# Performance work log

Hardware: AMD Instinct MI355X
Metric: run time of the kernel (lower is better)

Reference implementation:

```python
import jax, jax.numpy as jnp
import numpy as np

HEAD = 8
DIM_HEAD = 64
EPS = 1e-5  # torch GroupNorm default


def group_norm(x, w, b, groups, eps=EPS):
    # x: [B, C, H, W]; normalize per (group, spatial)
    B, C, H, W = x.shape
    xg = x.reshape(B, groups, C // groups, H, W)
    mu = xg.mean(axis=(2, 3, 4), keepdims=True)
    var = xg.var(axis=(2, 3, 4), keepdims=True)
    xn = ((xg - mu) / jnp.sqrt(var + eps)).reshape(B, C, H, W)
    return xn * w[None, :, None, None] + b[None, :, None, None]


def setup_inputs() -> dict:
    key = jax.random.key(0)
    ks = jax.random.split(key, 4)
    dim = 256
    hidden = HEAD * DIM_HEAD  # 512
    x = jax.random.normal(ks[0], (16, dim, 64, 64), dtype=jnp.float32)
    qkv_w = jax.random.normal(ks[1], (hidden * 3, dim), dtype=jnp.float32) * 0.02
    out_w = jax.random.normal(ks[2], (dim, hidden), dtype=jnp.float32) * 0.02
    out_b = jnp.zeros((dim,), dtype=jnp.float32)
    gn1_w = jnp.ones((dim,), dtype=jnp.float32)
    gn1_b = jnp.zeros((dim,), dtype=jnp.float32)
    gn2_w = jnp.ones((dim,), dtype=jnp.float32)
    gn2_b = jnp.zeros((dim,), dtype=jnp.float32)
    return {"x": x, "gn1_w": gn1_w, "gn1_b": gn1_b, "qkv_w": qkv_w,
            "out_w": out_w, "out_b": out_b, "gn2_w": gn2_w, "gn2_b": gn2_b}


def reference(x, gn1_w, gn1_b, qkv_w, out_w, out_b, gn2_w, gn2_b):
    B, C, I, J = x.shape
    groups = C // 8
    scale = DIM_HEAD ** -0.5
    n = I * J

    xn = group_norm(x, gn1_w, gn1_b, groups)
    # 1x1 conv == channel matmul: [B,3*hidden,I,J]
    qkv = jnp.einsum('bchw,oc->bohw', xn, qkv_w)
    q, k, v = jnp.split(qkv, 3, axis=1)

    def to_heads(t):  # [B, h*f, I, J] -> [B, h, f, n]
        return t.reshape(B, HEAD, DIM_HEAD, n)

    q = jax.nn.softmax(to_heads(q), axis=-2) * scale  # softmax over feature dim
    k = jax.nn.softmax(to_heads(k), axis=-1)          # softmax over spatial dim
    v = to_heads(v)

    context = jnp.einsum('bhfm,bhem->bhfe', k, v)     # [B,h,f,e]
    attn = jnp.einsum('bhfe,bhfn->bhen', context, q)  # [B,h,e,n]
    out = attn.reshape(B, HEAD * DIM_HEAD, I, J)

    out = jnp.einsum('bchw,oc->bohw', out, out_w) + out_b[None, :, None, None]
    return group_norm(out, gn2_w, gn2_b, groups)
```

## Files before the change

kernel.cpp:

```cpp
#include <hip/hip_runtime.h>
#include <math.h>

#define NB   16
#define NC   256
#define NP   4096
#define NHD  8
#define FD   64
#define HID  512
#define OC3  1536
#define NG   32
#define CPG  8
#define GEPS 1e-5f

typedef __attribute__((ext_vector_type(8))) short bf16x8;
typedef __attribute__((ext_vector_type(4))) float f32x4;

#define MFMA_BF16(a, b, c) __builtin_amdgcn_mfma_f32_16x16x32_bf16(a, b, c, 0, 0, 0)

__device__ __forceinline__ uint bf16_rne(float v) {
    uint u = __float_as_uint(v);
    return (u + 0x7FFFu + ((u >> 16) & 1u)) >> 16;
}
__device__ __forceinline__ void split2(float v, uint& h, uint& l) {
    h = bf16_rne(v);
    l = bf16_rne(v - __uint_as_float(h << 16));
}
__device__ __forceinline__ void gload16(const void* g, void* l) {
    __builtin_amdgcn_global_load_lds(
        (const __attribute__((address_space(1))) void*)g,
        (__attribute__((address_space(3))) void*)l, 16, 0, 0);
}

__global__ __launch_bounds__(256) void gn_stats_kernel(const float* __restrict__ x,
                                                       float* __restrict__ mu,
                                                       float* __restrict__ rstd) {
    int bg = blockIdx.x;
    const float4* b4 = (const float4*)(x + (size_t)bg * CPG * NP);
    int t = threadIdx.x;
    float s = 0.f, sq = 0.f;
    #pragma unroll
    for (int i = 0; i < 32; ++i) {
        float4 v = b4[t + i * 256];
        s  += v.x + v.y + v.z + v.w;
        sq += v.x*v.x + v.y*v.y + v.z*v.z + v.w*v.w;
    }
    for (int off = 32; off; off >>= 1) { s += __shfl_down(s, off); sq += __shfl_down(sq, off); }
    __shared__ float ss[4], ssq[4];
    int wid = t >> 6, lane = t & 63;
    if (lane == 0) { ss[wid] = s; ssq[wid] = sq; }
    __syncthreads();
    if (t == 0) {
        float S  = ss[0] + ss[1] + ss[2] + ss[3];
        float SQ = ssq[0] + ssq[1] + ssq[2] + ssq[3];
        const float inv = 1.f / (float)(CPG * NP);
        float m = S * inv;
        float var = SQ * inv - m * m;
        mu[bg] = m;
        rstd[bg] = rsqrtf(var + GEPS);
    }
}

__global__ void gn1_coefs_kernel(const float* __restrict__ mu, const float* __restrict__ rstd,
                                 const float* __restrict__ w, const float* __restrict__ bias,
                                 float* __restrict__ ac, float* __restrict__ dc) {
    int i = blockIdx.x * 256 + threadIdx.x;
    if (i >= NB * NC) return;
    int b = i / NC, c = i % NC;
    int g = c / CPG;
    float m = mu[b * NG + g], r = rstd[b * NG + g];
    float a = r * w[c];
    ac[i] = a;
    dc[i] = bias[c] - m * a;
}

__global__ void wsplit_kernel(const float* __restrict__ w, ushort* __restrict__ wh,
                              ushort* __restrict__ wl) {
    int i = blockIdx.x * 256 + threadIdx.x;
    float4 v = ((const float4*)w)[i];
    uint h, l;
    ushort4 hv, lv;
    split2(v.x, h, l); hv.x = (ushort)h; lv.x = (ushort)l;
    split2(v.y, h, l); hv.y = (ushort)h; lv.y = (ushort)l;
    split2(v.z, h, l); hv.z = (ushort)h; lv.z = (ushort)l;
    split2(v.w, h, l); hv.w = (ushort)h; lv.w = (ushort)l;
    ((ushort4*)wh)[i] = hv;
    ((ushort4*)wl)[i] = lv;
}

__global__ __launch_bounds__(256) void xsplit_kernel(const float* __restrict__ x,
                                                     const float* __restrict__ ac,
                                                     const float* __restrict__ dc,
                                                     ushort* __restrict__ xTh,
                                                     ushort* __restrict__ xTl, int b0) {
    int z = blockIdx.z, bglob = b0 + z;
    int p0 = blockIdx.x * 64, c0 = blockIdx.y * 64;
    const float* xb = x + (size_t)bglob * NC * NP;
    __shared__ float T[64][72];
    int t = threadIdx.x;
    #pragma unroll
    for (int j = 0; j < 4; ++j) {
        int idx = t + j * 256;
        int r = idx >> 4, c4 = idx & 15;
        float4 v = *(const float4*)(xb + (size_t)(c0 + r) * NP + p0 + c4 * 4);
        float a = ac[bglob * NC + c0 + r], d = dc[bglob * NC + c0 + r];
        v.x = fmaf(v.x, a, d); v.y = fmaf(v.y, a, d);
        v.z = fmaf(v.z, a, d); v.w = fmaf(v.w, a, d);
        *(float4*)&T[r][c4 * 4] = v;
    }
    __syncthreads();
    int p = t >> 2, cseg = t & 3;
    size_t ob = ((size_t)z * NP + p0 + p) * NC + c0 + cseg * 16;
    #pragma unroll
    for (int half = 0; half < 2; ++half) {
        uint4 uh, ul;
        uint* ph = (uint*)&uh; uint* pl = (uint*)&ul;
        #pragma unroll
        for (int i = 0; i < 4; ++i) {
            int c = cseg * 16 + half * 8 + i * 2;
            uint h0, l0, h1, l1;
            split2(T[c][p], h0, l0);
            split2(T[c + 1][p], h1, l1);
            ph[i] = h0 | (h1 << 16);
            pl[i] = l0 | (l1 << 16);
        }
        *(uint4*)(xTh + ob + half * 8) = uh;
        *(uint4*)(xTl + ob + half * 8) = ul;
    }
}

__global__ __launch_bounds__(256) void gemm_q_kernel(
        const ushort* __restrict__ Ah, const ushort* __restrict__ Al,
        const ushort* __restrict__ Bhg, const ushort* __restrict__ Blg,
        ushort* __restrict__ qsTh) {
    __shared__ __align__(16) char smem[33280];
    const int z = blockIdx.z;
    const ushort* Bh = Bhg + (size_t)NP * NC * z;
    const ushort* Bl = Blg + (size_t)NP * NC * z;

    const int t = threadIdx.x;
    const int w = t >> 6, l = t & 63;
    const int wr = w >> 1, wc = w & 1;
    const int m0 = blockIdx.y * 128, n0 = blockIdx.x * 128;
    const int l15 = l & 15, kb = l >> 4;

    f32x4 acc[4][4];
    #pragma unroll
    for (int i = 0; i < 4; ++i)
        #pragma unroll
        for (int j = 0; j < 4; ++j)
            acc[i][j] = (f32x4){0.f, 0.f, 0.f, 0.f};

    for (int k0 = 0; k0 < NC; k0 += 32) {
        #pragma unroll
        for (int j = 0; j < 2; ++j) {
            int idx = t + j * 256;
            int m = idx & 127, s = idx >> 7;
            size_t goA = (size_t)(m0 + m) * NC + k0 + s * 8;
            size_t goB = (size_t)(n0 + m) * NC + k0 + s * 8;
            int lo = idx * 16;
            gload16(Ah + goA, smem + lo);
            gload16(Al + goA, smem + 8192 + lo);
            gload16(Bh + goB, smem + 16384 + lo);
            gload16(Bl + goB, smem + 24576 + lo);
        }
        __syncthreads();
        bf16x8 ah[4], al[4];
        #pragma unroll
        for (int fi = 0; fi < 4; ++fi) {
            int off = (kb * 128 + wr * 64 + fi * 16 + l15) * 16;
            ah[fi] = *(const bf16x8*)(smem + off);
            al[fi] = *(const bf16x8*)(smem + 8192 + off);
        }
        #pragma unroll
        for (int fj = 0; fj < 4; ++fj) {
            int off = (kb * 128 + wc * 64 + fj * 16 + l15) * 16;
            bf16x8 bh = *(const bf16x8*)(smem + 16384 + off);
            bf16x8 bl = *(const bf16x8*)(smem + 24576 + off);
            #pragma unroll
            for (int fi = 0; fi < 4; ++fi) {
                acc[fi][fj] = MFMA_BF16(ah[fi], bh, acc[fi][fj]);
                acc[fi][fj] = MFMA_BF16(al[fi], bh, acc[fi][fj]);
                acc[fi][fj] = MFMA_BF16(ah[fi], bl, acc[fi][fj]);
            }
        }
        __syncthreads();
    }

    uint* Tq = (uint*)smem;
    #pragma unroll
    for (int half = 0; half < 2; ++half) {
        if (wc == half) {
            #pragma unroll
            for (int fj = 0; fj < 4; ++fj) {
                float ex[16];
                float cs = 0.f;
                #pragma unroll
                for (int fi = 0; fi < 4; ++fi)
                    #pragma unroll
                    for (int r = 0; r < 4; ++r) {
                        float e = __expf(acc[fi][fj][r]);
                        ex[fi * 4 + r] = e;
                        cs += e;
                    }
                cs += __shfl_xor(cs, 16);
                cs += __shfl_xor(cs, 32);
                float inv = 0.125f / cs;
                int p_loc = fj * 16 + l15;
                #pragma unroll
                for (int fi = 0; fi < 4; ++fi)
                    #pragma unroll
                    for (int r = 0; r < 4; ++r) {
                        uint hb = bf16_rne(ex[fi * 4 + r] * inv);
                        Tq[p_loc * 130 + wr * 64 + fi * 16 + kb * 4 + r] = hb << 16;
                    }
            }
        }
        __syncthreads();
        int p = t >> 2, seg = t & 3;
        size_t ob = ((size_t)z * NP + n0 + half * 64 + p) * HID + m0 + seg * 32;
        #pragma unroll
        for (int c = 0; c < 4; ++c) {
            uint4 H;
            uint* hp = (uint*)&H;
            #pragma unroll
            for (int i = 0; i < 4; ++i) {
                uint u0 = Tq[p * 130 + seg * 32 + c * 8 + 2 * i];
                uint u1 = Tq[p * 130 + seg * 32 + c * 8 + 2 * i + 1];
                hp[i] = (u0 >> 16) | (u1 & 0xffff0000u);
            }
            *(uint4*)(qsTh + ob + c * 8) = H;
        }
        __syncthreads();
    }
}

__global__ __launch_bounds__(512, 4) void kv_ctx_kernel(
        const ushort* __restrict__ Wh, const ushort* __restrict__ Wl,
        const ushort* __restrict__ Bhg, const ushort* __restrict__ Blg,
        float* __restrict__ ctxp, float* __restrict__ kspart) {
    __shared__ __align__(16) char smem[69632];
    const int z = blockIdx.z;
    const int h = blockIdx.y;
    const int tile = blockIdx.x;
    const int n0 = tile * 128;
    const ushort* Bh = Bhg + (size_t)NP * NC * z;
    const ushort* Bl = Blg + (size_t)NP * NC * z;

    const int t = threadIdx.x;
    const int w = t >> 6, l = t & 63;
    const int wr = w >> 2, wc = w & 3;
    const int l15 = l & 15, kb = l >> 4;

    ushort* ekh = (ushort*)smem;
    ushort* ekl = ekh + 64 * 136;
    ushort* vh_ = ekl + 64 * 136;
    ushort* vl_ = vh_ + 64 * 136;

    f32x4 acc[4][2];
    #pragma unroll
    for (int i = 0; i < 4; ++i)
        #pragma unroll
        for (int j = 0; j < 2; ++j)
            acc[i][j] = (f32x4){0.f, 0.f, 0.f, 0.f};

    for (int k0 = 0; k0 < NC; k0 += 32) {
        {
            int idx = t;
            int m = idx & 127, s = idx >> 7;
            int grow = 512 + h * 64 + (m & 63) + ((m >> 6) << 9);
            size_t goA = (size_t)grow * NC + k0 + s * 8;
            size_t goB = (size_t)(n0 + m) * NC + k0 + s * 8;
            int lo = idx * 16;
            gload16(Wh + goA, smem + lo);
            gload16(Wl + goA, smem + 8192 + lo);
            gload16(Bh + goB, smem + 16384 + lo);
            gload16(Bl + goB, smem + 24576 + lo);
        }
        __syncthreads();
        bf16x8 ah[4], al[4];
        #pragma unroll
        for (int fi = 0; fi < 4; ++fi) {
            int off = (kb * 128 + wr * 64 + fi * 16 + l15) * 16;
            ah[fi] = *(const bf16x8*)(smem + off);
            al[fi] = *(const bf16x8*)(smem + 8192 + off);
        }
        #pragma unroll
        for (int fj = 0; fj < 2; ++fj) {
            int off = (kb * 128 + wc * 32 + fj * 16 + l15) * 16;
            bf16x8 bh = *(const bf16x8*)(smem + 16384 + off);
            bf16x8 bl = *(const bf16x8*)(smem + 24576 + off);
            #pragma unroll
            for (int fi = 0; fi < 4; ++fi) {
                acc[fi][fj] = MFMA_BF16(ah[fi], bh, acc[fi][fj]);
                acc[fi][fj] = MFMA_BF16(al[fi], bh, acc[fi][fj]);
                acc[fi][fj] = MFMA_BF16(ah[fi], bl, acc[fi][fj]);
            }
        }
        __syncthreads();
    }

    #pragma unroll
    for (int fi = 0; fi < 4; ++fi) {
        #pragma unroll
        for (int r = 0; r < 4; ++r) {
            int row = fi * 16 + kb * 4 + r;
            float rs = 0.f;
            #pragma unroll
            for (int fj = 0; fj < 2; ++fj) {
                float v = acc[fi][fj][r];
                float e = (wr == 0) ? __expf(v) : v;
                rs += e;
                uint hb, lb;
                split2(e, hb, lb);
                int P = wc * 32 + fj * 16 + l15;
                if (wr == 0) { ekh[row * 136 + P] = (ushort)hb; ekl[row * 136 + P] = (ushort)lb; }
                else         { vh_[row * 136 + P] = (ushort)hb; vl_[row * 136 + P] = (ushort)lb; }
            }
            if (wr == 0) {
                rs += __shfl_xor(rs, 1); rs += __shfl_xor(rs, 2);
                rs += __shfl_xor(rs, 4); rs += __shfl_xor(rs, 8);
                if (l15 == 0)
                    kspart[((size_t)z * HID + h * 64 + row) * 128 + tile * 4 + wc] = rs;
            }
        }
    }
    __syncthreads();

    f32x4 c2[2];
    c2[0] = (f32x4){0.f, 0.f, 0.f, 0.f};
    c2[1] = (f32x4){0.f, 0.f, 0.f, 0.f};
    const int cr0 = (w >> 2) * 32;
    const int cc0 = (w & 3) * 16;
    #pragma unroll
    for (int ks = 0; ks < 4; ++ks) {
        bf16x8 a_h[2], a_l[2];
        #pragma unroll
        for (int i = 0; i < 2; ++i) {
            int offa = (cr0 + i * 16 + l15) * 136 + ks * 32 + kb * 8;
            a_h[i] = *(const bf16x8*)(ekh + offa);
            a_l[i] = *(const bf16x8*)(ekl + offa);
        }
        int offb = (cc0 + l15) * 136 + ks * 32 + kb * 8;
        bf16x8 b_h = *(const bf16x8*)(vh_ + offb);
        bf16x8 b_l = *(const bf16x8*)(vl_ + offb);
        #pragma unroll
        for (int i = 0; i < 2; ++i) {
            c2[i] = MFMA_BF16(a_h[i], b_h, c2[i]);
            c2[i] = MFMA_BF16(a_l[i], b_h, c2[i]);
            c2[i] = MFMA_BF16(a_h[i], b_l, c2[i]);
        }
    }
    float* outp = ctxp + (((size_t)z * NHD + h) * 32 + tile) * 4096;
    #pragma unroll
    for (int i = 0; i < 2; ++i)
        #pragma unroll
        for (int r = 0; r < 4; ++r)
            outp[(size_t)(cr0 + i * 16 + kb * 4 + r) * 64 + cc0 + l15] = c2[i][r];
}

__global__ void ksum_reduce_kernel(const float* __restrict__ kspart,
                                   float* __restrict__ ksum, int n) {
    int i = blockIdx.x * 256 + threadIdx.x;
    if (i >= n) return;
    float s = 0.f;
    #pragma unroll
    for (int j = 0; j < 128; ++j) s += kspart[(size_t)i * 128 + j];
    ksum[i] = s;
}

__global__ __launch_bounds__(256) void fold_kernel(const float* __restrict__ out_w,
                                                   const float* __restrict__ ctxp,
                                                   const float* __restrict__ ksum,
                                                   ushort* __restrict__ w2h,
                                                   ushort* __restrict__ w2l) {
    int h = blockIdx.x, z = blockIdx.y;
    __shared__ float Cs[FD][FD];
    int t = threadIdx.x;
    const float* pbase = ctxp + ((size_t)z * NHD + h) * 32 * 4096;
    #pragma unroll
    for (int j = 0; j < 16; ++j) {
        int idx = t + j * 256;
        float s = 0.f;
        #pragma unroll
        for (int p8 = 0; p8 < 32; ++p8) s += pbase[(size_t)p8 * 4096 + idx];
        ((float*)Cs)[idx] = s;
    }
    __syncthreads();
    float wr[64];
    const float* wrow = out_w + (size_t)t * HID + h * FD;
    #pragma unroll
    for (int e = 0; e < 64; ++e) wr[e] = wrow[e];
    size_t ob = ((size_t)z * NC + t) * HID + h * FD;
    for (int f = 0; f < 64; ++f) {
        float sacc = 0.f;
        #pragma unroll
        for (int e = 0; e < 64; ++e) sacc = fmaf(wr[e], Cs[f][e], sacc);
        float v = sacc / ksum[(size_t)z * HID + h * FD + f];
        uint hb, lb;
        split2(v, hb, lb);
        w2h[ob + f] = (ushort)hb;
        w2l[ob + f] = (ushort)lb;
    }
}

__global__ __launch_bounds__(256) void gemm_out_kernel(
        const ushort* __restrict__ Ahg, const ushort* __restrict__ Alg,
        const ushort* __restrict__ Bhg,
        const float* __restrict__ bias, float* __restrict__ outg,
        float2* __restrict__ gn2part, int b0) {
    __shared__ __align__(16) char smem[24576];
    const int z = blockIdx.z, bglob = b0 + z;
    const ushort* Ah = Ahg + (size_t)NC * HID * z;
    const ushort* Al = Alg + (size_t)NC * HID * z;
    const ushort* Bh = Bhg + (size_t)NP * HID * z;
    float* C = outg + (size_t)bglob * NC * NP;

    const int t = threadIdx.x;
    const int w = t >> 6, l = t & 63;
    const int wr = w >> 1, wc = w & 1;
    const int m0 = blockIdx.y * 128, n0 = blockIdx.x * 128;
    const int l15 = l & 15, kb = l >> 4;

    f32x4 acc[4][4];
    #pragma unroll
    for (int i = 0; i < 4; ++i)
        #pragma unroll
        for (int j = 0; j < 4; ++j)
            acc[i][j] = (f32x4){0.f, 0.f, 0.f, 0.f};

    for (int k0 = 0; k0 < HID; k0 += 32) {
        #pragma unroll
        for (int j = 0; j < 2; ++j) {
            int idx = t + j * 256;
            int m = idx & 127, s = idx >> 7;
            size_t goA = (size_t)(m0 + m) * HID + k0 + s * 8;
            size_t goB = (size_t)(n0 + m) * HID + k0 + s * 8;
            int lo = idx * 16;
            gload16(Ah + goA, smem + lo);
            gload16(Al + goA, smem + 8192 + lo);
            gload16(Bh + goB, smem + 16384 + lo);
        }
        __syncthreads();
        bf16x8 ah[4], al[4];
        #pragma unroll
        for (int fi = 0; fi < 4; ++fi) {
            int off = (kb * 128 + wr * 64 + fi * 16 + l15) * 16;
            ah[fi] = *(const bf16x8*)(smem + off);
            al[fi] = *(const bf16x8*)(smem + 8192 + off);
        }
        #pragma unroll
        for (int fj = 0; fj < 4; ++fj) {
            int off = (kb * 128 + wc * 64 + fj * 16 + l15) * 16;
            bf16x8 bh = *(const bf16x8*)(smem + 16384 + off);
            #pragma unroll
            for (int fi = 0; fi < 4; ++fi) {
                acc[fi][fj] = MFMA_BF16(ah[fi], bh, acc[fi][fj]);
                acc[fi][fj] = MFMA_BF16(al[fi], bh, acc[fi][fj]);
            }
        }
        __syncthreads();
    }

    float gs[4] = {0.f, 0.f, 0.f, 0.f}, gq[4] = {0.f, 0.f, 0.f, 0.f};
    #pragma unroll
    for (int fi = 0; fi < 4; ++fi) {
        int mbase = m0 + wr * 64 + fi * 16 + kb * 4;
        #pragma unroll
        for (int fj = 0; fj < 4; ++fj) {
            int n = n0 + wc * 64 + fj * 16 + l15;
            #pragma unroll
            for (int r = 0; r < 4; ++r) {
                float v = acc[fi][fj][r] + bias[mbase + r];
                C[(size_t)(mbase + r) * NP + n] = v;
                gs[fi] += v;
                gq[fi] += v * v;
            }
        }
    }
    #pragma unroll
    for (int fi = 0; fi < 4; ++fi) {
        #pragma unroll
        for (int d = 1; d <= 16; d <<= 1) {
            gs[fi] += __shfl_xor(gs[fi], d);
            gq[fi] += __shfl_xor(gq[fi], d);
        }
    }
    if (l15 == 0 && (kb & 1) == 0) {
        #pragma unroll
        for (int fi = 0; fi < 4; ++fi) {
            int g = ((m0 + wr * 64) >> 3) + fi * 2 + (kb >> 1);
            float2 pv; pv.x = gs[fi]; pv.y = gq[fi];
            gn2part[(((size_t)bglob * NG + g) << 6) + blockIdx.x * 2 + wc] = pv;
        }
    }
}

__global__ void gn2_reduce_kernel(const float2* __restrict__ gn2part,
                                  float* __restrict__ mu, float* __restrict__ rstd) {
    int i = blockIdx.x * 256 + threadIdx.x;
    if (i >= NB * NG) return;
    float s = 0.f, q = 0.f;
    #pragma unroll
    for (int j = 0; j < 64; ++j) {
        float2 p = gn2part[((size_t)i << 6) + j];
        s += p.x; q += p.y;
    }
    const float inv = 1.f / (float)(CPG * NP);
    float m = s * inv;
    float var = q * inv - m * m;
    mu[i] = m;
    rstd[i] = rsqrtf(var + GEPS);
}

__global__ void gn2_apply_kernel(float* __restrict__ out, const float* __restrict__ mu,
                                 const float* __restrict__ rstd, const float* __restrict__ w,
                                 const float* __restrict__ bias) {
    int i = blockIdx.x * 256 + threadIdx.x;
    float4* p = (float4*)out;
    float4 v = p[i];
    size_t e0 = (size_t)i * 4;
    int cidx = (int)((e0 / NP) % NC);
    int bg   = (int)(e0 / ((size_t)CPG * NP));
    float m = mu[bg], r = rstd[bg];
    float a = r * w[cidx];
    float d = bias[cidx] - m * a;
    v.x = fmaf(v.x, a, d); v.y = fmaf(v.y, a, d);
    v.z = fmaf(v.z, a, d); v.w = fmaf(v.w, a, d);
    p[i] = v;
}

extern "C" void kernel_launch(void* const* d_in, const int* in_sizes, int n_in,
                              void* d_out, int out_size, void* d_ws, size_t ws_size,
                              hipStream_t stream) {
    const float* x     = (const float*)d_in[0];
    const float* gn1_w = (const float*)d_in[1];
    const float* gn1_b = (const float*)d_in[2];
    const float* qkv_w = (const float*)d_in[3];
    const float* out_w = (const float*)d_in[4];
    const float* out_b = (const float*)d_in[5];
    const float* gn2_w = (const float*)d_in[6];
    const float* gn2_b = (const float*)d_in[7];
    float* out = (float*)d_out;

    auto need = [](int cb) -> size_t {
        size_t tot = 0;
        auto al = [&](size_t b) { tot = (tot + b + 255) & ~(size_t)255; };
        al((size_t)cb * NP * NC * 2);  al((size_t)cb * NP * NC * 2);
        al((size_t)cb * NP * HID * 2);
        al((size_t)cb * NHD * 32 * FD * FD * 4);
        al((size_t)cb * HID * 128 * 4);
        al((size_t)cb * HID * 4);
        al((size_t)cb * NC * HID * 2); al((size_t)cb * NC * HID * 2);
        al((size_t)OC3 * NC * 2); al((size_t)OC3 * NC * 2);
        al((size_t)2 * NB * NC * 4);
        al((size_t)4 * NB * NG * 4);
        al((size_t)NB * NG * 64 * 8);
        return tot;
    };
    int CB = 1;
    {
        const int cands[5] = {16, 8, 4, 2, 1};
        for (int i = 0; i < 5; ++i) if (need(cands[i]) <= ws_size) { CB = cands[i]; break; }
    }

    char* base = (char*)d_ws;
    size_t off = 0;
    auto carve = [&](size_t b) -> char* {
        char* p = base + off;
        off = (off + b + 255) & ~(size_t)255;
        return p;
    };
    ushort* xTh  = (ushort*)carve((size_t)CB * NP * NC * 2);
    ushort* xTl  = (ushort*)carve((size_t)CB * NP * NC * 2);
    ushort* qsTh = (ushort*)carve((size_t)CB * NP * HID * 2);
    float*  ctxp = (float*) carve((size_t)CB * NHD * 32 * FD * FD * 4);
    float*  kspart = (float*)carve((size_t)CB * HID * 128 * 4);
    float*  ksum = (float*) carve((size_t)CB * HID * 4);
    ushort* w2h  = (ushort*)carve((size_t)CB * NC * HID * 2);
    ushort* w2l  = (ushort*)carve((size_t)CB * NC * HID * 2);
    ushort* Wqh  = (ushort*)carve((size_t)OC3 * NC * 2);
    ushort* Wql  = (ushort*)carve((size_t)OC3 * NC * 2);
    float*  ac   = (float*) carve((size_t)2 * NB * NC * 4);
    float*  dc   = ac + (size_t)NB * NC;
    float*  mu1  = (float*) carve((size_t)4 * NB * NG * 4);
    float*  rstd1 = mu1 + NB * NG;
    float*  mu2   = rstd1 + NB * NG;
    float*  rstd2 = mu2 + NB * NG;
    float2* gn2part = (float2*)carve((size_t)NB * NG * 64 * 8);

    gn_stats_kernel<<<NB * NG, 256, 0, stream>>>(x, mu1, rstd1);
    gn1_coefs_kernel<<<16, 256, 0, stream>>>(mu1, rstd1, gn1_w, gn1_b, ac, dc);
    wsplit_kernel<<<OC3 * NC / 1024, 256, 0, stream>>>(qkv_w, Wqh, Wql);

    for (int b0 = 0; b0 < NB; b0 += CB) {
        xsplit_kernel<<<dim3(NP / 64, NC / 64, CB), 256, 0, stream>>>(x, ac, dc, xTh, xTl, b0);
        kv_ctx_kernel<<<dim3(NP / 128, NHD, CB), 512, 0, stream>>>(Wqh, Wql, xTh, xTl, ctxp, kspart);
        ksum_reduce_kernel<<<(CB * HID + 255) / 256, 256, 0, stream>>>(kspart, ksum, CB * HID);
        gemm_q_kernel<<<dim3(NP / 128, 4, CB), 256, 0, stream>>>(Wqh, Wql, xTh, xTl, qsTh);
        fold_kernel<<<dim3(NHD, CB), 256, 0, stream>>>(out_w, ctxp, ksum, w2h, w2l);
        gemm_out_kernel<<<dim3(NP / 128, 2, CB), 256, 0, stream>>>(
            w2h, w2l, qsTh, out_b, out, gn2part, b0);
    }

    gn2_reduce_kernel<<<2, 256, 0, stream>>>(gn2part, mu2, rstd2);
    gn2_apply_kernel<<<16384, 256, 0, stream>>>(out, mu2, rstd2, gn2_w, gn2_b);
}
```

Before: 487.4 us.

## Merge Q projection GEMM into the KV context kernel as extra grid blocks

Removes the separate gemm_q_kernel launch and folds its work into the kv_ctx kernel: blocks with blockIdx.y >= NHD compute the Q projection plus feature softmax, the rest compute K/V context. The Q path is restructured to 512 threads with 128x128 tiles and one epilogue pass instead of two halves, with the smem row stride changed to 136. This cuts a launch and lets Q and KV work share one grid, improving fill. The cost is that the Q path now runs under the 512-thread, 4-block launch bounds and the larger shared-memory footprint of the KV kernel.

```diff
diff --git a/kernel.cpp b/kernel.cpp
--- a/kernel.cpp
+++ b/kernel.cpp
@@ -128,119 +128,13 @@
     }
 }
 
-__global__ __launch_bounds__(256) void gemm_q_kernel(
-        const ushort* __restrict__ Ah, const ushort* __restrict__ Al,
-        const ushort* __restrict__ Bhg, const ushort* __restrict__ Blg,
-        ushort* __restrict__ qsTh) {
-    __shared__ __align__(16) char smem[33280];
-    const int z = blockIdx.z;
-    const ushort* Bh = Bhg + (size_t)NP * NC * z;
-    const ushort* Bl = Blg + (size_t)NP * NC * z;
-
-    const int t = threadIdx.x;
-    const int w = t >> 6, l = t & 63;
-    const int wr = w >> 1, wc = w & 1;
-    const int m0 = blockIdx.y * 128, n0 = blockIdx.x * 128;
-    const int l15 = l & 15, kb = l >> 4;
-
-    f32x4 acc[4][4];
-    #pragma unroll
-    for (int i = 0; i < 4; ++i)
-        #pragma unroll
-        for (int j = 0; j < 4; ++j)
-            acc[i][j] = (f32x4){0.f, 0.f, 0.f, 0.f};
-
-    for (int k0 = 0; k0 < NC; k0 += 32) {
-        #pragma unroll
-        for (int j = 0; j < 2; ++j) {
-            int idx = t + j * 256;
-            int m = idx & 127, s = idx >> 7;
-            size_t goA = (size_t)(m0 + m) * NC + k0 + s * 8;
-            size_t goB = (size_t)(n0 + m) * NC + k0 + s * 8;
-            int lo = idx * 16;
-            gload16(Ah + goA, smem + lo);
-            gload16(Al + goA, smem + 8192 + lo);
-            gload16(Bh + goB, smem + 16384 + lo);
-            gload16(Bl + goB, smem + 24576 + lo);
-        }
-        __syncthreads();
-        bf16x8 ah[4], al[4];
-        #pragma unroll
-        for (int fi = 0; fi < 4; ++fi) {
-            int off = (kb * 128 + wr * 64 + fi * 16 + l15) * 16;
-            ah[fi] = *(const bf16x8*)(smem + off);
-            al[fi] = *(const bf16x8*)(smem + 8192 + off);
-        }
-        #pragma unroll
-        for (int fj = 0; fj < 4; ++fj) {
-            int off = (kb * 128 + wc * 64 + fj * 16 + l15) * 16;
-            bf16x8 bh = *(const bf16x8*)(smem + 16384 + off);
-            bf16x8 bl = *(const bf16x8*)(smem + 24576 + off);
-            #pragma unroll
-            for (int fi = 0; fi < 4; ++fi) {
-                acc[fi][fj] = MFMA_BF16(ah[fi], bh, acc[fi][fj]);
-                acc[fi][fj] = MFMA_BF16(al[fi], bh, acc[fi][fj]);
-                acc[fi][fj] = MFMA_BF16(ah[fi], bl, acc[fi][fj]);
-            }
-        }
-        __syncthreads();
-    }
-
-    uint* Tq = (uint*)smem;
-    #pragma unroll
-    for (int half = 0; half < 2; ++half) {
-        if (wc == half) {
-            #pragma unroll
-            for (int fj = 0; fj < 4; ++fj) {
-                float ex[16];
-                float cs = 0.f;
-                #pragma unroll
-                for (int fi = 0; fi < 4; ++fi)
-                    #pragma unroll
-                    for (int r = 0; r < 4; ++r) {
-                        float e = __expf(acc[fi][fj][r]);
-                        ex[fi * 4 + r] = e;
-                        cs += e;
-                    }
-                cs += __shfl_xor(cs, 16);
-                cs += __shfl_xor(cs, 32);
-                float inv = 0.125f / cs;
-                int p_loc = fj * 16 + l15;
-                #pragma unroll
-                for (int fi = 0; fi < 4; ++fi)
-                    #pragma unroll
-                    for (int r = 0; r < 4; ++r) {
-                        uint hb = bf16_rne(ex[fi * 4 + r] * inv);
-                        Tq[p_loc * 130 + wr * 64 + fi * 16 + kb * 4 + r] = hb << 16;
-                    }
-            }
-        }
-        __syncthreads();
-        int p = t >> 2, seg = t & 3;
-        size_t ob = ((size_t)z * NP + n0 + half * 64 + p) * HID + m0 + seg * 32;
-        #pragma unroll
-        for (int c = 0; c < 4; ++c) {
-            uint4 H;
-            uint* hp = (uint*)&H;
-            #pragma unroll
-            for (int i = 0; i < 4; ++i) {
-                uint u0 = Tq[p * 130 + seg * 32 + c * 8 + 2 * i];
-                uint u1 = Tq[p * 130 + seg * 32 + c * 8 + 2 * i + 1];
-                hp[i] = (u0 >> 16) | (u1 & 0xffff0000u);
-            }
-            *(uint4*)(qsTh + ob + c * 8) = H;
-        }
-        __syncthreads();
-    }
-}
-
-__global__ __launch_bounds__(512, 4) void kv_ctx_kernel(
+__global__ __launch_bounds__(512, 4) void kvq_kernel(
         const ushort* __restrict__ Wh, const ushort* __restrict__ Wl,
         const ushort* __restrict__ Bhg, const ushort* __restrict__ Blg,
-        float* __restrict__ ctxp, float* __restrict__ kspart) {
+        float* __restrict__ ctxp, float* __restrict__ kspart,
+        ushort* __restrict__ qsTh) {
     __shared__ __align__(16) char smem[69632];
     const int z = blockIdx.z;
-    const int h = blockIdx.y;
     const int tile = blockIdx.x;
     const int n0 = tile * 128;
     const ushort* Bh = Bhg + (size_t)NP * NC * z;
@@ -251,11 +145,6 @@
     const int wr = w >> 2, wc = w & 3;
     const int l15 = l & 15, kb = l >> 4;
 
-    ushort* ekh = (ushort*)smem;
-    ushort* ekl = ekh + 64 * 136;
-    ushort* vh_ = ekl + 64 * 136;
-    ushort* vl_ = vh_ + 64 * 136;
-
     f32x4 acc[4][2];
     #pragma unroll
     for (int i = 0; i < 4; ++i)
@@ -263,99 +152,185 @@
         for (int j = 0; j < 2; ++j)
             acc[i][j] = (f32x4){0.f, 0.f, 0.f, 0.f};
 
-    for (int k0 = 0; k0 < NC; k0 += 32) {
-        {
-            int idx = t;
-            int m = idx & 127, s = idx >> 7;
-            int grow = 512 + h * 64 + (m & 63) + ((m >> 6) << 9);
-            size_t goA = (size_t)grow * NC + k0 + s * 8;
-            size_t goB = (size_t)(n0 + m) * NC + k0 + s * 8;
-            int lo = idx * 16;
-            gload16(Wh + goA, smem + lo);
-            gload16(Wl + goA, smem + 8192 + lo);
-            gload16(Bh + goB, smem + 16384 + lo);
-            gload16(Bl + goB, smem + 24576 + lo);
+    if (blockIdx.y < NHD) {
+        const int h = blockIdx.y;
+        ushort* ekh = (ushort*)smem;
+        ushort* ekl = ekh + 64 * 136;
+        ushort* vh_ = ekl + 64 * 136;
+        ushort* vl_ = vh_ + 64 * 136;
+
+        for (int k0 = 0; k0 < NC; k0 += 32) {
+            {
+                int idx = t;
+                int m = idx & 127, s = idx >> 7;
+                int grow = 512 + h * 64 + (m & 63) + ((m >> 6) << 9);
+                size_t goA = (size_t)grow * NC + k0 + s * 8;
+                size_t goB = (size_t)(n0 + m) * NC + k0 + s * 8;
+                int lo = idx * 16;
+                gload16(Wh + goA, smem + lo);
+                gload16(Wl + goA, smem + 8192 + lo);
+                gload16(Bh + goB, smem + 16384 + lo);
+                gload16(Bl + goB, smem + 24576 + lo);
+            }
+            __syncthreads();
+            bf16x8 ah[4], al[4];
+            #pragma unroll
+            for (int fi = 0; fi < 4; ++fi) {
+                int off = (kb * 128 + wr * 64 + fi * 16 + l15) * 16;
+                ah[fi] = *(const bf16x8*)(smem + off);
+                al[fi] = *(const bf16x8*)(smem + 8192 + off);
+            }
+            #pragma unroll
+            for (int fj = 0; fj < 2; ++fj) {
+                int off = (kb * 128 + wc * 32 + fj * 16 + l15) * 16;
+                bf16x8 bh = *(const bf16x8*)(smem + 16384 + off);
+                bf16x8 bl = *(const bf16x8*)(smem + 24576 + off);
+                #pragma unroll
+                for (int fi = 0; fi < 4; ++fi) {
+                    acc[fi][fj] = MFMA_BF16(ah[fi], bh, acc[fi][fj]);
+                    acc[fi][fj] = MFMA_BF16(al[fi], bh, acc[fi][fj]);
+                    acc[fi][fj] = MFMA_BF16(ah[fi], bl, acc[fi][fj]);
+                }
+            }
+            __syncthreads();
+        }
+
+        #pragma unroll
+        for (int fi = 0; fi < 4; ++fi) {
+            #pragma unroll
+            for (int r = 0; r < 4; ++r) {
+                int row = fi * 16 + kb * 4 + r;
+                float rs = 0.f;
+                #pragma unroll
+                for (int fj = 0; fj < 2; ++fj) {
+                    float v = acc[fi][fj][r];
+                    float e = (wr == 0) ? __expf(v) : v;
+                    rs += e;
+                    uint hb, lb;
+                    split2(e, hb, lb);
+                    int P = wc * 32 + fj * 16 + l15;
+                    if (wr == 0) { ekh[row * 136 + P] = (ushort)hb; ekl[row * 136 + P] = (ushort)lb; }
+                    else         { vh_[row * 136 + P] = (ushort)hb; vl_[row * 136 + P] = (ushort)lb; }
+                }
+                if (wr == 0) {
+                    rs += __shfl_xor(rs, 1); rs += __shfl_xor(rs, 2);
+                    rs += __shfl_xor(rs, 4); rs += __shfl_xor(rs, 8);
+                    if (l15 == 0)
+                        kspart[((size_t)z * HID + h * 64 + row) * 128 + tile * 4 + wc] = rs;
+                }
+            }
         }
         __syncthreads();
-        bf16x8 ah[4], al[4];
-        #pragma unroll
-        for (int fi = 0; fi < 4; ++fi) {
-            int off = (kb * 128 + wr * 64 + fi * 16 + l15) * 16;
-            ah[fi] = *(const bf16x8*)(smem + off);
-            al[fi] = *(const bf16x8*)(smem + 8192 + off);
-        }
+
+        f32x4 c2[2];
+        c2[0] = (f32x4){0.f, 0.f, 0.f, 0.f};
+        c2[1] = (f32x4){0.f, 0.f, 0.f, 0.f};
+        const int cr0 = (w >> 2) * 32;
+        const int cc0 = (w & 3) * 16;
+        #pragma unroll
+        for (int ks = 0; ks < 4; ++ks) {
+            bf16x8 a_h[2], a_l[2];
+            #pragma unroll
+            for (int i = 0; i < 2; ++i) {
+                int offa = (cr0 + i * 16 + l15) * 136 + ks * 32 + kb * 8;
+                a_h[i] = *(const bf16x8*)(ekh + offa);
+                a_l[i] = *(const bf16x8*)(ekl + offa);
+            }
+            int offb = (cc0 + l15) * 136 + ks * 32 + kb * 8;
+            bf16x8 b_h = *(const bf16x8*)(vh_ + offb);
+            bf16x8 b_l = *(const bf16x8*)(vl_ + offb);
+            #pragma unroll
+            for (int i = 0; i < 2; ++i) {
+                c2[i] = MFMA_BF16(a_h[i], b_h, c2[i]);
+                c2[i] = MFMA_BF16(a_l[i], b_h, c2[i]);
+                c2[i] = MFMA_BF16(a_h[i], b_l, c2[i]);
+            }
+        }
+        float* outp = ctxp + (((size_t)z * NHD + h) * 32 + tile) * 4096;
+        #pragma unroll
+        for (int i = 0; i < 2; ++i)
+            #pragma unroll
+            for (int r = 0; r < 4; ++r)
+                outp[(size_t)(cr0 + i * 16 + kb * 4 + r) * 64 + cc0 + l15] = c2[i][r];
+    } else {
+        const int m0 = (blockIdx.y - NHD) * 128;
+
+        for (int k0 = 0; k0 < NC; k0 += 32) {
+            {
+                int idx = t;
+                int m = idx & 127, s = idx >> 7;
+                size_t goA = (size_t)(m0 + m) * NC + k0 + s * 8;
+                size_t goB = (size_t)(n0 + m) * NC + k0 + s * 8;
+                int lo = idx * 16;
+                gload16(Wh + goA, smem + lo);
+                gload16(Wl + goA, smem + 8192 + lo);
+                gload16(Bh + goB, smem + 16384 + lo);
+                gload16(Bl + goB, smem + 24576 + lo);
+            }
+            __syncthreads();
+            bf16x8 ah[4], al[4];
+            #pragma unroll
+            for (int fi = 0; fi < 4; ++fi) {
+                int off = (kb * 128 + wr * 64 + fi * 16 + l15) * 16;
+                ah[fi] = *(const bf16x8*)(smem + off);
+                al[fi] = *(const bf16x8*)(smem + 8192 + off);
+            }
+            #pragma unroll
+            for (int fj = 0; fj < 2; ++fj) {
+                int off = (kb * 128 + wc * 32 + fj * 16 + l15) * 16;
+                bf16x8 bh = *(const bf16x8*)(smem + 16384 + off);
+                bf16x8 bl = *(const bf16x8*)(smem + 24576 + off);
+                #pragma unroll
+                for (int fi = 0; fi < 4; ++fi) {
+                    acc[fi][fj] = MFMA_BF16(ah[fi], bh, acc[fi][fj]);
+                    acc[fi][fj] = MFMA_BF16(al[fi], bh, acc[fi][fj]);
+                    acc[fi][fj] = MFMA_BF16(ah[fi], bl, acc[fi][fj]);
+                }
+            }
+            __syncthreads();
+        }
+
+        uint* Tq = (uint*)smem;
         #pragma unroll
         for (int fj = 0; fj < 2; ++fj) {
-            int off = (kb * 128 + wc * 32 + fj * 16 + l15) * 16;
-            bf16x8 bh = *(const bf16x8*)(smem + 16384 + off);
-            bf16x8 bl = *(const bf16x8*)(smem + 24576 + off);
-            #pragma unroll
-            for (int fi = 0; fi < 4; ++fi) {
-                acc[fi][fj] = MFMA_BF16(ah[fi], bh, acc[fi][fj]);
-                acc[fi][fj] = MFMA_BF16(al[fi], bh, acc[fi][fj]);
-                acc[fi][fj] = MFMA_BF16(ah[fi], bl, acc[fi][fj]);
-            }
+            float ex[16];
+            float cs = 0.f;
+            #pragma unroll
+            for (int fi = 0; fi < 4; ++fi)
+                #pragma unroll
+                for (int r = 0; r < 4; ++r) {
+                    float e = __expf(acc[fi][fj][r]);
+                    ex[fi * 4 + r] = e;
+                    cs += e;
+                }
+            cs += __shfl_xor(cs, 16);
+            cs += __shfl_xor(cs, 32);
+            float inv = 0.125f / cs;
+            int p_loc = wc * 32 + fj * 16 + l15;
+            #pragma unroll
+            for (int fi = 0; fi < 4; ++fi)
+                #pragma unroll
+                for (int r = 0; r < 4; ++r) {
+                    uint hb = bf16_rne(ex[fi * 4 + r] * inv);
+                    Tq[p_loc * 136 + wr * 64 + fi * 16 + kb * 4 + r] = hb << 16;
+                }
         }
         __syncthreads();
-    }
-
-    #pragma unroll
-    for (int fi = 0; fi < 4; ++fi) {
-        #pragma unroll
-        for (int r = 0; r < 4; ++r) {
-            int row = fi * 16 + kb * 4 + r;
-            float rs = 0.f;
-            #pragma unroll
-            for (int fj = 0; fj < 2; ++fj) {
-                float v = acc[fi][fj][r];
-                float e = (wr == 0) ? __expf(v) : v;
-                rs += e;
-                uint hb, lb;
-                split2(e, hb, lb);
-                int P = wc * 32 + fj * 16 + l15;
-                if (wr == 0) { ekh[row * 136 + P] = (ushort)hb; ekl[row * 136 + P] = (ushort)lb; }
-                else         { vh_[row * 136 + P] = (ushort)hb; vl_[row * 136 + P] = (ushort)lb; }
-            }
-            if (wr == 0) {
-                rs += __shfl_xor(rs, 1); rs += __shfl_xor(rs, 2);
-                rs += __shfl_xor(rs, 4); rs += __shfl_xor(rs, 8);
-                if (l15 == 0)
-                    kspart[((size_t)z * HID + h * 64 + row) * 128 + tile * 4 + wc] = rs;
-            }
-        }
-    }
-    __syncthreads();
-
-    f32x4 c2[2];
-    c2[0] = (f32x4){0.f, 0.f, 0.f, 0.f};
-    c2[1] = (f32x4){0.f, 0.f, 0.f, 0.f};
-    const int cr0 = (w >> 2) * 32;
-    const int cc0 = (w & 3) * 16;
-    #pragma unroll
-    for (int ks = 0; ks < 4; ++ks) {
-        bf16x8 a_h[2], a_l[2];
-        #pragma unroll
-        for (int i = 0; i < 2; ++i) {
-            int offa = (cr0 + i * 16 + l15) * 136 + ks * 32 + kb * 8;
-            a_h[i] = *(const bf16x8*)(ekh + offa);
-            a_l[i] = *(const bf16x8*)(ekl + offa);
-        }
-        int offb = (cc0 + l15) * 136 + ks * 32 + kb * 8;
-        bf16x8 b_h = *(const bf16x8*)(vh_ + offb);
-        bf16x8 b_l = *(const bf16x8*)(vl_ + offb);
-        #pragma unroll
-        for (int i = 0; i < 2; ++i) {
-            c2[i] = MFMA_BF16(a_h[i], b_h, c2[i]);
-            c2[i] = MFMA_BF16(a_l[i], b_h, c2[i]);
-            c2[i] = MFMA_BF16(a_h[i], b_l, c2[i]);
-        }
-    }
-    float* outp = ctxp + (((size_t)z * NHD + h) * 32 + tile) * 4096;
-    #pragma unroll
-    for (int i = 0; i < 2; ++i)
-        #pragma unroll
-        for (int r = 0; r < 4; ++r)
-            outp[(size_t)(cr0 + i * 16 + kb * 4 + r) * 64 + cc0 + l15] = c2[i][r];
+        int p = t >> 2, seg = t & 3;
+        size_t ob = ((size_t)z * NP + n0 + p) * HID + m0 + seg * 32;
+        #pragma unroll
+        for (int c = 0; c < 4; ++c) {
+            uint4 H;
+            uint* hp = (uint*)&H;
+            #pragma unroll
+            for (int i = 0; i < 4; ++i) {
+                uint u0 = Tq[p * 136 + seg * 32 + c * 8 + 2 * i];
+                uint u1 = Tq[p * 136 + seg * 32 + c * 8 + 2 * i + 1];
+                hp[i] = (u0 >> 16) | (u1 & 0xffff0000u);
+            }
+            *(uint4*)(qsTh + ob + c * 8) = H;
+        }
+    }
 }
 
 __global__ void ksum_reduce_kernel(const float* __restrict__ kspart,
@@ -594,9 +569,9 @@
 
     for (int b0 = 0; b0 < NB; b0 += CB) {
         xsplit_kernel<<<dim3(NP / 64, NC / 64, CB), 256, 0, stream>>>(x, ac, dc, xTh, xTl, b0);
-        kv_ctx_kernel<<<dim3(NP / 128, NHD, CB), 512, 0, stream>>>(Wqh, Wql, xTh, xTl, ctxp, kspart);
+        kvq_kernel<<<dim3(NP / 128, NHD + 4, CB), 512, 0, stream>>>(
+            Wqh, Wql, xTh, xTl, ctxp, kspart, qsTh);
         ksum_reduce_kernel<<<(CB * HID + 255) / 256, 256, 0, stream>>>(kspart, ksum, CB * HID);
-        gemm_q_kernel<<<dim3(NP / 128, 4, CB), 256, 0, stream>>>(Wqh, Wql, xTh, xTl, qsTh);
         fold_kernel<<<dim3(NHD, CB), 256, 0, stream>>>(out_w, ctxp, ksum, w2h, w2l);
         gemm_out_kernel<<<dim3(NP / 128, 2, CB), 256, 0, stream>>>(
             w2h, w2l, qsTh, out_b, out, gn2part, b0);
```

After: 474.0 us, median of 2. 1.03x faster.
